# Optimization experiments

Hardware: AMD Instinct MI355X
Metric: run time of the kernel (lower is better)

## Reference

```python
import jax, jax.numpy as jnp
import numpy as np

HIDDEN = 1024
INTER = 4096
NUM_EXPERTS = 8
TOP_K = 2
LN_EPS = 1e-5


def setup_inputs() -> dict:
    key = jax.random.key(0)
    ks = jax.random.split(key, 8)
    B, S = 4, 2048
    scale = 0.02
    return {
        "hidden_states": jax.random.normal(ks[0], (B, S, HIDDEN), dtype=jnp.float32),
        "ln_scale": jnp.ones((HIDDEN,), jnp.float32),
        "ln_bias": jnp.zeros((HIDDEN,), jnp.float32),
        "router_w": jax.random.normal(ks[1], (NUM_EXPERTS, HIDDEN), jnp.float32) * scale,
        "router_b": jnp.zeros((NUM_EXPERTS,), jnp.float32),
        "up_w": jax.random.normal(ks[2], (NUM_EXPERTS, INTER, HIDDEN), jnp.float32) * scale,
        "up_b": jnp.zeros((NUM_EXPERTS, INTER), jnp.float32),
        "down_w": jax.random.normal(ks[3], (NUM_EXPERTS, HIDDEN, INTER), jnp.float32) * scale,
        "down_b": jnp.zeros((NUM_EXPERTS, HIDDEN), jnp.float32),
    }


def reference(hidden_states, ln_scale, ln_bias, router_w, router_b, up_w, up_b, down_w, down_b):
    B, S, H = hidden_states.shape
    x = hidden_states.reshape(-1, H)  # [T, H]

    # router LayerNorm (eps=1e-5, affine)
    mu = jnp.mean(x, axis=-1, keepdims=True)
    var = jnp.var(x, axis=-1, keepdims=True)
    xn = (x - mu) * jax.lax.rsqrt(var + LN_EPS) * ln_scale + ln_bias

    logits = xn @ router_w.T + router_b                # [T, E]
    top_w, top_idx = jax.lax.top_k(logits, TOP_K)      # [T, K]
    top_w = jax.nn.softmax(top_w.astype(jnp.float32), axis=-1).astype(x.dtype)

    out = jnp.zeros_like(x)
    for e in range(NUM_EXPERTS):
        # per-token combine weight for expert e (0 if not selected)
        gate = jnp.sum(jnp.where(top_idx == e, top_w, 0.0), axis=-1)  # [T]
        # expert MLP (dropout is identity in eval); GELU is exact (erf) as nn.GELU default
        h = jax.nn.gelu(x @ up_w[e].T + up_b[e], approximate=False)
        h = h @ down_w[e].T + down_b[e]
        out = out + gate[:, None] * h
    return out.reshape(B, S, H)
```

## Files before the change

kernel.cpp:

```cpp
#include <hip/hip_runtime.h>
#include <math.h>

#define HIDDEN 1024
#define INTER 4096
#define NE 8

typedef __bf16 bf16;
typedef __bf16 bf16x8 __attribute__((ext_vector_type(8)));
typedef float f32x4 __attribute__((ext_vector_type(4)));

#define WS_CTRL   ((size_t)0)
#define WS_PERM   ((size_t)256)
#define WS_GATES  ((size_t)65792)
#define WS_EIDX   ((size_t)131328)
#define WS_EGATE  ((size_t)196864)
#define WS_XB     ((size_t)262400)
#define WS_UPWB   ((size_t)17039616)
#define WS_DOWNWB ((size_t)84148480)
#define WS_H      ((size_t)151257344)
#define WS_T2S    ((size_t)285475072)
#define WS_Y      WS_UPWB

__device__ __forceinline__ void async_copy16(const void* g, void* l) {
  __builtin_amdgcn_global_load_lds((const __attribute__((address_space(1))) void*)g,
                                   (__attribute__((address_space(3))) void*)l, 16, 0, 0);
}

__device__ __forceinline__ int xcd_remap(int orig, int nwg) {
  int q = nwg >> 3, r = nwg & 7;
  int xcd = orig & 7, idx = orig >> 3;
  int base = (xcd < r) ? xcd * (q + 1) : r * (q + 1) + (xcd - r) * q;
  return base + idx;
}

__device__ __forceinline__ float gelu_erf(float v) {
  float x = v * 0.70710678118654752440f;
  float ax = fabsf(x);
  float t = __builtin_amdgcn_rcpf(fmaf(0.3275911f, ax, 1.0f));
  float p = fmaf(t, 1.061405429f, -1.453152027f);
  p = fmaf(p, t, 1.421413741f);
  p = fmaf(p, t, -0.284496736f);
  p = fmaf(p, t, 0.254829592f);
  p = p * t;
  float e = __expf(-x * x);
  float er = 1.0f - p * e;
  er = copysignf(er, x);
  return 0.5f * v * (1.0f + er);
}

__global__ void cvt_kernel(const float* __restrict__ w, bf16* __restrict__ wb, int n4) {
  int i = blockIdx.x * blockDim.x + threadIdx.x;
  int stride = gridDim.x * blockDim.x;
  for (; i < n4; i += stride) {
    float4 v = ((const float4*)w)[i];
    union { bf16 b[4]; uint2 u; } cv;
    cv.b[0] = (bf16)v.x; cv.b[1] = (bf16)v.y; cv.b[2] = (bf16)v.z; cv.b[3] = (bf16)v.w;
    ((uint2*)wb)[i] = cv.u;
  }
}

__global__ __launch_bounds__(256)
void router_kernel(const float* __restrict__ x, const float* __restrict__ lns,
                   const float* __restrict__ lnb, const float* __restrict__ rw,
                   const float* __restrict__ rb, bf16* __restrict__ xb,
                   int* __restrict__ eidx, float* __restrict__ egate) {
  const int lane = threadIdx.x & 63;
  const int wid = threadIdx.x >> 6;
  const int t = blockIdx.x * 4 + wid;
  const float4* xr = (const float4*)(x + (size_t)t * HIDDEN);
  float4 v[4];
  float s = 0.f, ss = 0.f;
#pragma unroll
  for (int q = 0; q < 4; ++q) {
    v[q] = xr[q * 64 + lane];
    s += v[q].x + v[q].y + v[q].z + v[q].w;
    ss += v[q].x * v[q].x + v[q].y * v[q].y + v[q].z * v[q].z + v[q].w * v[q].w;
  }
#pragma unroll
  for (int o = 32; o; o >>= 1) { s += __shfl_xor(s, o, 64); ss += __shfl_xor(ss, o, 64); }
  const float mu = s * (1.f / HIDDEN);
  const float rstd = rsqrtf(ss * (1.f / HIDDEN) - mu * mu + 1e-5f);
  float acc[NE] = {};
#pragma unroll
  for (int q = 0; q < 4; ++q) {
    int i4 = q * 64 + lane;
    float4 xv = v[q];
    float4 sc = ((const float4*)lns)[i4];
    float4 bi = ((const float4*)lnb)[i4];
    float4 xn;
    xn.x = (xv.x - mu) * rstd * sc.x + bi.x;
    xn.y = (xv.y - mu) * rstd * sc.y + bi.y;
    xn.z = (xv.z - mu) * rstd * sc.z + bi.z;
    xn.w = (xv.w - mu) * rstd * sc.w + bi.w;
#pragma unroll
    for (int e2 = 0; e2 < NE; ++e2) {
      float4 w = ((const float4*)(rw + e2 * HIDDEN))[i4];
      acc[e2] += xn.x * w.x + xn.y * w.y + xn.z * w.z + xn.w * w.w;
    }
    union { bf16 b[4]; uint2 u; } cv;
    cv.b[0] = (bf16)xv.x; cv.b[1] = (bf16)xv.y; cv.b[2] = (bf16)xv.z; cv.b[3] = (bf16)xv.w;
    *(uint2*)&xb[(size_t)t * HIDDEN + i4 * 4] = cv.u;
  }
#pragma unroll
  for (int e2 = 0; e2 < NE; ++e2)
#pragma unroll
    for (int o = 32; o; o >>= 1) acc[e2] += __shfl_xor(acc[e2], o, 64);
  if (lane == 0) {
    float b0 = -1e30f, b1 = -1e30f; int i0 = 0, i1 = 0;
#pragma unroll
    for (int e2 = 0; e2 < NE; ++e2) {
      float lv = acc[e2] + rb[e2];
      if (lv > b0) { b1 = b0; i1 = i0; b0 = lv; i0 = e2; }
      else if (lv > b1) { b1 = lv; i1 = e2; }
    }
    float ex = expf(b1 - b0);
    float g0 = 1.f / (1.f + ex);
    float g1 = ex * g0;
    eidx[t * 2] = i0; eidx[t * 2 + 1] = i1;
    egate[t * 2] = g0; egate[t * 2 + 1] = g1;
  }
}

__global__ __launch_bounds__(256)
void hist_kernel(const int* __restrict__ eidx, int* __restrict__ cnt) {
  __shared__ int h8[NE];
  if (threadIdx.x < NE) h8[threadIdx.x] = 0;
  __syncthreads();
  int i = (blockIdx.x * 256 + threadIdx.x) * 4;
#pragma unroll
  for (int k = 0; k < 4; ++k) atomicAdd(&h8[eidx[i + k]], 1);
  __syncthreads();
  if (threadIdx.x < NE) atomicAdd(&cnt[threadIdx.x], h8[threadIdx.x]);
}

__global__ void scan_kernel(const int* cnt, int* offs) {
  if (threadIdx.x == 0 && blockIdx.x == 0) {
    int a = 0;
    for (int e = 0; e < NE; ++e) { offs[e] = a; a += cnt[e]; }
    offs[NE] = a;
  }
}

__global__ __launch_bounds__(256)
void scatter_kernel(const int* __restrict__ eidx, const float* __restrict__ egate,
                    const int* __restrict__ offs, int* __restrict__ fill,
                    int* __restrict__ perm, float* __restrict__ gates,
                    int* __restrict__ t2s) {
  __shared__ int h8[NE], base8[NE];
  if (threadIdx.x < NE) h8[threadIdx.x] = 0;
  __syncthreads();
  int i = (blockIdx.x * 256 + threadIdx.x) * 4;
  int ee[4], rk[4];
#pragma unroll
  for (int k = 0; k < 4; ++k) { ee[k] = eidx[i + k]; rk[k] = atomicAdd(&h8[ee[k]], 1); }
  __syncthreads();
  if (threadIdx.x < NE) base8[threadIdx.x] = atomicAdd(&fill[threadIdx.x], h8[threadIdx.x]);
  __syncthreads();
#pragma unroll
  for (int k = 0; k < 4; ++k) {
    int entry = i + k;
    int slot = offs[ee[k]] + base8[ee[k]] + rk[k];
    perm[slot] = entry >> 1;
    gates[slot] = egate[entry];
    t2s[entry] = slot;
  }
}

#define READ_A(hh, cb) { \
  _Pragma("unroll") for (int ii = 0; ii < 4; ++ii) \
  _Pragma("unroll") for (int ks = 0; ks < 2; ++ks) { \
    int r_ = wr * 128 + (hh) * 64 + ii * 16 + l15; \
    af[ii][ks] = *(const bf16x8*)&sA[cb][r_ * 64 + (((ks * 4 + l16) ^ (r_ & 7)) * 8)]; \
  } }

#define READ_B(jh, cb) { \
  _Pragma("unroll") for (int jj = 0; jj < 2; ++jj) \
  _Pragma("unroll") for (int ks = 0; ks < 2; ++ks) { \
    int n_ = wc * 64 + ((jh) * 2 + jj) * 16 + l15; \
    bfr[jh][jj][ks] = *(const bf16x8*)&sB[cb][n_ * 64 + (((ks * 4 + l16) ^ (n_ & 7)) * 8)]; \
  } }

#define STAGE_A(ha, nb) { \
  async_copy16(ga[ha][0], &sA[nb][la[ha][0]]); \
  async_copy16(ga[ha][1], &sA[nb][la[ha][1]]); \
  ga[ha][0] += 64; ga[ha][1] += 64; }

#define STAGE_B(hb, nb) { \
  async_copy16(gb[hb][0], &sB[nb][lb[hb][0]]); \
  async_copy16(gb[hb][1], &sB[nb][lb[hb][1]]); \
  gb[hb][0] += 64; gb[hb][1] += 64; }

#define MFMA_CLUSTER(I0, JH) \
  __builtin_amdgcn_s_barrier(); \
  asm volatile("s_waitcnt lgkmcnt(0)" ::: "memory"); \
  __builtin_amdgcn_sched_barrier(0); \
  __builtin_amdgcn_s_setprio(1); \
  { _Pragma("unroll") for (int ii = 0; ii < 4; ++ii) \
    _Pragma("unroll") for (int jj = 0; jj < 2; ++jj) \
    _Pragma("unroll") for (int ks = 0; ks < 2; ++ks) \
      acc[(I0) + ii][(JH) * 2 + jj] = __builtin_amdgcn_mfma_f32_16x16x32_bf16( \
          af[ii][ks], bfr[JH][jj][ks], acc[(I0) + ii][(JH) * 2 + jj], 0, 0, 0); } \
  __builtin_amdgcn_s_setprio(0); \
  __builtin_amdgcn_sched_barrier(0); \
  __builtin_amdgcn_s_barrier();

#define VMW(n) asm volatile("s_waitcnt vmcnt(" #n ")" ::: "memory");

#define GEMM8_MAIN_LOOP(NT) \
  STAGE_A(0, 0); STAGE_B(0, 0); STAGE_B(1, 0); STAGE_A(1, 0); \
  VMW(4); \
  __builtin_amdgcn_s_barrier(); \
  for (int t = 0; t < (NT) - 1; ++t) { \
    const int cb = t & 1, nb = cb ^ 1; \
    READ_A(0, cb); READ_B(0, cb); \
    STAGE_A(0, nb); \
    VMW(4); \
    MFMA_CLUSTER(0, 0); \
    READ_B(1, cb); \
    STAGE_B(0, nb); \
    VMW(4); \
    MFMA_CLUSTER(0, 1); \
    READ_A(1, cb); \
    STAGE_B(1, nb); \
    MFMA_CLUSTER(4, 1); \
    STAGE_A(1, nb); \
    VMW(4); \
    MFMA_CLUSTER(4, 0); \
  } \
  { \
    const int cb = ((NT) - 1) & 1; \
    READ_A(0, cb); READ_B(0, cb); \
    VMW(0); \
    MFMA_CLUSTER(0, 0); \
    READ_B(1, cb); \
    MFMA_CLUSTER(0, 1); \
    READ_A(1, cb); \
    MFMA_CLUSTER(4, 1); \
    MFMA_CLUSTER(4, 0); \
  }

#define UP_CT (INTER / 256)
#define UP_RT 32
__global__ __launch_bounds__(512, 2)
void up_gemm8(const bf16* __restrict__ xb, const bf16* __restrict__ wb,
              const float* __restrict__ upb, const int* __restrict__ perm,
              const int* __restrict__ offs, bf16* __restrict__ h) {
  const int wgid = xcd_remap(blockIdx.x, UP_CT * UP_RT * NE);
  const int ct = wgid % UP_CT;
  const int rt = (wgid / UP_CT) % UP_RT;
  const int e  = wgid / (UP_CT * UP_RT);
  const int pbase = offs[e];
  const int ne = offs[e + 1] - pbase;
  if (rt * 256 >= ne) return;
  __shared__ __align__(16) bf16 sA[2][256 * 64];
  __shared__ __align__(16) bf16 sB[2][256 * 64];
  const int tid = threadIdx.x;
  const int lane = tid & 63;
  const int wid = tid >> 6;
  const int wr = wid >> 2;
  const int wc = wid & 3;
  const int l15 = lane & 15, l16 = lane >> 4;

  const bf16* ga[2][2]; int la[2][2];
  const bf16* gb[2][2]; int lb[2][2];
  {
    int tr = tid >> 3, tc = tid & 7;
#pragma unroll
    for (int hh = 0; hh < 2; ++hh)
#pragma unroll
      for (int l = 0; l < 2; ++l) {
        int arow = hh * 64 + tr + l * 128;
        int asch = tc ^ (arow & 7);
        int ar = rt * 256 + arow; if (ar > ne - 1) ar = ne - 1;
        int tok = perm[pbase + ar];
        ga[hh][l] = xb + (size_t)tok * HIDDEN + asch * 8;
        la[hh][l] = arow * 64 + tc * 8;
        int rl = l * 64 + tr;
        int brow = hh * 32 + (rl & 31) + (rl >> 5) * 64;
        int bsch = tc ^ (brow & 7);
        int bn = ct * 256 + brow;
        gb[hh][l] = wb + ((size_t)e * INTER + bn) * HIDDEN + bsch * 8;
        lb[hh][l] = brow * 64 + tc * 8;
      }
  }

  f32x4 acc[8][4] = {};
  bf16x8 af[4][2];
  bf16x8 bfr[2][2][2];

  GEMM8_MAIN_LOOP(HIDDEN / 64)

#pragma unroll
  for (int j4 = 0; j4 < 4; ++j4) {
    int c = ct * 256 + wc * 64 + j4 * 16 + l15;
    float bias = upb[e * INTER + c];
#pragma unroll
    for (int i8 = 0; i8 < 8; ++i8) {
#pragma unroll
      for (int tq = 0; tq < 4; ++tq) {
        int r = rt * 256 + wr * 128 + i8 * 16 + l16 * 4 + tq;
        if (r < ne) {
          float v = gelu_erf(acc[i8][j4][tq] + bias);
          h[(size_t)(pbase + r) * INTER + c] = (bf16)v;
        }
      }
    }
  }
}

#define DN_CT (HIDDEN / 256)
#define DN_RT 32
__global__ __launch_bounds__(512, 2)
void down_gemm8(const bf16* __restrict__ hh_, const bf16* __restrict__ wb,
                const float* __restrict__ dnb, const float* __restrict__ gates,
                const int* __restrict__ offs, float* __restrict__ y) {
  const int wgid = xcd_remap(blockIdx.x, DN_CT * DN_RT * NE);
  const int ct = wgid % DN_CT;
  const int rt = (wgid / DN_CT) % DN_RT;
  const int e  = wgid / (DN_CT * DN_RT);
  const int pbase = offs[e];
  const int ne = offs[e + 1] - pbase;
  if (rt * 256 >= ne) return;
  __shared__ __align__(16) bf16 sA[2][256 * 64];
  __shared__ __align__(16) bf16 sB[2][256 * 64];
  const int tid = threadIdx.x;
  const int lane = tid & 63;
  const int wid = tid >> 6;
  const int wr = wid >> 2;
  const int wc = wid & 3;
  const int l15 = lane & 15, l16 = lane >> 4;

  const bf16* ga[2][2]; int la[2][2];
  const bf16* gb[2][2]; int lb[2][2];
  {
    int tr = tid >> 3, tc = tid & 7;
#pragma unroll
    for (int hhp = 0; hhp < 2; ++hhp)
#pragma unroll
      for (int l = 0; l < 2; ++l) {
        int arow = hhp * 64 + tr + l * 128;
        int asch = tc ^ (arow & 7);
        int ar = rt * 256 + arow; if (ar > ne - 1) ar = ne - 1;
        ga[hhp][l] = hh_ + (size_t)(pbase + ar) * INTER + asch * 8;
        la[hhp][l] = arow * 64 + tc * 8;
        int rl = l * 64 + tr;
        int brow = hhp * 32 + (rl & 31) + (rl >> 5) * 64;
        int bsch = tc ^ (brow & 7);
        int bn = ct * 256 + brow;
        gb[hhp][l] = wb + ((size_t)e * HIDDEN + bn) * INTER + bsch * 8;
        lb[hhp][l] = brow * 64 + tc * 8;
      }
  }

  f32x4 acc[8][4] = {};
  bf16x8 af[4][2];
  bf16x8 bfr[2][2][2];

  GEMM8_MAIN_LOOP(INTER / 64)

  float bias[4];
#pragma unroll
  for (int j4 = 0; j4 < 4; ++j4)
    bias[j4] = dnb[e * HIDDEN + ct * 256 + wc * 64 + j4 * 16 + l15];

#pragma unroll
  for (int i8 = 0; i8 < 8; ++i8) {
#pragma unroll
    for (int tq = 0; tq < 4; ++tq) {
      int r = rt * 256 + wr * 128 + i8 * 16 + l16 * 4 + tq;
      if (r < ne) {
        int slot = pbase + r;
        float gt = gates[slot];
#pragma unroll
        for (int j4 = 0; j4 < 4; ++j4) {
          int c = ct * 256 + wc * 64 + j4 * 16 + l15;
          y[(size_t)slot * HIDDEN + c] = gt * (acc[i8][j4][tq] + bias[j4]);
        }
      }
    }
  }
}

__global__ __launch_bounds__(256)
void combine_kernel(const float* __restrict__ y, const int* __restrict__ t2s,
                    float* __restrict__ out) {
  int t = blockIdx.x;
  int s0 = t2s[2 * t], s1 = t2s[2 * t + 1];
  const float4* a = (const float4*)(y + (size_t)s0 * HIDDEN);
  const float4* b = (const float4*)(y + (size_t)s1 * HIDDEN);
  float4* o = (float4*)(out + (size_t)t * HIDDEN);
  int c = threadIdx.x;
  float4 va = a[c], vb = b[c];
  o[c] = make_float4(va.x + vb.x, va.y + vb.y, va.z + vb.z, va.w + vb.w);
}

extern "C" void kernel_launch(void* const* d_in, const int* in_sizes, int n_in,
                              void* d_out, int out_size, void* d_ws, size_t ws_size,
                              hipStream_t stream) {
  const float* x   = (const float*)d_in[0];
  const float* lns = (const float*)d_in[1];
  const float* lnb = (const float*)d_in[2];
  const float* rw  = (const float*)d_in[3];
  const float* rb  = (const float*)d_in[4];
  const float* upw = (const float*)d_in[5];
  const float* upb = (const float*)d_in[6];
  const float* dww = (const float*)d_in[7];
  const float* dwb = (const float*)d_in[8];
  float* out = (float*)d_out;

  char* ws = (char*)d_ws;
  int* ctrl   = (int*)(ws + WS_CTRL);
  int* cnt    = ctrl;
  int* fill   = ctrl + 8;
  int* offs   = ctrl + 16;
  int* perm   = (int*)(ws + WS_PERM);
  float* gates = (float*)(ws + WS_GATES);
  int* eidx   = (int*)(ws + WS_EIDX);
  float* egate = (float*)(ws + WS_EGATE);
  bf16* xb    = (bf16*)(ws + WS_XB);
  bf16* upwb  = (bf16*)(ws + WS_UPWB);
  bf16* dwwb  = (bf16*)(ws + WS_DOWNWB);
  bf16* h     = (bf16*)(ws + WS_H);
  int* t2s    = (int*)(ws + WS_T2S);
  float* y    = (float*)(ws + WS_Y);

  const int T = in_sizes[0] / HIDDEN;

  hipMemsetAsync(ctrl, 0, 256, stream);

  cvt_kernel<<<4096, 256, 0, stream>>>(upw, upwb, NE * INTER * HIDDEN / 4);
  cvt_kernel<<<4096, 256, 0, stream>>>(dww, dwwb, NE * HIDDEN * INTER / 4);
  router_kernel<<<T / 4, 256, 0, stream>>>(x, lns, lnb, rw, rb, xb, eidx, egate);
  hist_kernel<<<(2 * T) / 1024, 256, 0, stream>>>(eidx, cnt);
  scan_kernel<<<1, 64, 0, stream>>>(cnt, offs);
  scatter_kernel<<<(2 * T) / 1024, 256, 0, stream>>>(eidx, egate, offs, fill, perm, gates, t2s);

  up_gemm8<<<UP_CT * UP_RT * NE, 512, 0, stream>>>(xb, upwb, upb, perm, offs, h);
  down_gemm8<<<DN_CT * DN_RT * NE, 512, 0, stream>>>(h, dwwb, dwb, gates, offs, y);
  combine_kernel<<<T, 256, 0, stream>>>(y, t2s, out);
}
```

Measured before the change: 624.2 us.

## Double-buffer MFMA fragments and overlap LDS reads with MFMA clusters

Restructures the GEMM main loop so A/B fragments go into separate register buffers (af0/af1, b0/b1). LDS reads for the next sub-block are issued while the current MFMA block runs, and the next tile's first fragments are prefetched at the end of each iteration. Each MFMA cluster now uses one barrier instead of two and drops the explicit lgkmcnt(0) wait, and the vmcnt waits are loosened from 4 to 2. The aim is to hide LDS latency and cut barrier overhead. The cost is more VGPRs under launch_bounds(512,2), and the looser waits and barriers add a risk of races on the double-buffered shared tiles.

```diff
diff --git a/kernel.cpp b/kernel.cpp
--- a/kernel.cpp
+++ b/kernel.cpp
@@ -166,18 +166,18 @@
   }
 }
 
-#define READ_A(hh, cb) { \
+#define READ_A_TO(dst, hh, cb) { \
   _Pragma("unroll") for (int ii = 0; ii < 4; ++ii) \
   _Pragma("unroll") for (int ks = 0; ks < 2; ++ks) { \
     int r_ = wr * 128 + (hh) * 64 + ii * 16 + l15; \
-    af[ii][ks] = *(const bf16x8*)&sA[cb][r_ * 64 + (((ks * 4 + l16) ^ (r_ & 7)) * 8)]; \
+    dst[ii][ks] = *(const bf16x8*)&sA[cb][r_ * 64 + (((ks * 4 + l16) ^ (r_ & 7)) * 8)]; \
   } }
 
-#define READ_B(jh, cb) { \
+#define READ_B_TO(dst, jh, cb) { \
   _Pragma("unroll") for (int jj = 0; jj < 2; ++jj) \
   _Pragma("unroll") for (int ks = 0; ks < 2; ++ks) { \
     int n_ = wc * 64 + ((jh) * 2 + jj) * 16 + l15; \
-    bfr[jh][jj][ks] = *(const bf16x8*)&sB[cb][n_ * 64 + (((ks * 4 + l16) ^ (n_ & 7)) * 8)]; \
+    dst[jj][ks] = *(const bf16x8*)&sB[cb][n_ * 64 + (((ks * 4 + l16) ^ (n_ & 7)) * 8)]; \
   } }
 
 #define STAGE_A(ha, nb) { \
@@ -190,53 +190,58 @@
   async_copy16(gb[hb][1], &sB[nb][lb[hb][1]]); \
   gb[hb][0] += 64; gb[hb][1] += 64; }
 
-#define MFMA_CLUSTER(I0, JH) \
-  __builtin_amdgcn_s_barrier(); \
-  asm volatile("s_waitcnt lgkmcnt(0)" ::: "memory"); \
-  __builtin_amdgcn_sched_barrier(0); \
+#define MFMA_BLK(I0, JH, A, B) \
   __builtin_amdgcn_s_setprio(1); \
   { _Pragma("unroll") for (int ii = 0; ii < 4; ++ii) \
     _Pragma("unroll") for (int jj = 0; jj < 2; ++jj) \
     _Pragma("unroll") for (int ks = 0; ks < 2; ++ks) \
       acc[(I0) + ii][(JH) * 2 + jj] = __builtin_amdgcn_mfma_f32_16x16x32_bf16( \
-          af[ii][ks], bfr[JH][jj][ks], acc[(I0) + ii][(JH) * 2 + jj], 0, 0, 0); } \
-  __builtin_amdgcn_s_setprio(0); \
-  __builtin_amdgcn_sched_barrier(0); \
-  __builtin_amdgcn_s_barrier();
+          A[ii][ks], B[jj][ks], acc[(I0) + ii][(JH) * 2 + jj], 0, 0, 0); } \
+  __builtin_amdgcn_s_setprio(0);
 
 #define VMW(n) asm volatile("s_waitcnt vmcnt(" #n ")" ::: "memory");
+#define BAR() { __builtin_amdgcn_s_barrier(); __builtin_amdgcn_sched_barrier(0); }
 
 #define GEMM8_MAIN_LOOP(NT) \
   STAGE_A(0, 0); STAGE_B(0, 0); STAGE_B(1, 0); STAGE_A(1, 0); \
-  VMW(4); \
-  __builtin_amdgcn_s_barrier(); \
+  VMW(2); \
+  BAR(); \
+  READ_A_TO(af0, 0, 0); READ_B_TO(b0, 0, 0); \
   for (int t = 0; t < (NT) - 1; ++t) { \
     const int cb = t & 1, nb = cb ^ 1; \
-    READ_A(0, cb); READ_B(0, cb); \
+     \
+    READ_B_TO(b1, 1, cb); \
     STAGE_A(0, nb); \
-    VMW(4); \
-    MFMA_CLUSTER(0, 0); \
-    READ_B(1, cb); \
+    VMW(2); \
+    MFMA_BLK(0, 0, af0, b0); \
+    BAR(); \
+     \
+    READ_A_TO(af1, 1, cb); \
     STAGE_B(0, nb); \
-    VMW(4); \
-    MFMA_CLUSTER(0, 1); \
-    READ_A(1, cb); \
+    MFMA_BLK(0, 1, af0, b1); \
+    BAR(); \
+     \
     STAGE_B(1, nb); \
-    MFMA_CLUSTER(4, 1); \
+    MFMA_BLK(4, 1, af1, b1); \
+    BAR(); \
+     \
     STAGE_A(1, nb); \
-    VMW(4); \
-    MFMA_CLUSTER(4, 0); \
+    VMW(2); \
+    MFMA_BLK(4, 0, af1, b0); \
+    BAR(); \
+     \
+    READ_A_TO(af0, 0, nb); READ_B_TO(b0, 0, nb); \
   } \
-  { \
+  {  \
     const int cb = ((NT) - 1) & 1; \
-    READ_A(0, cb); READ_B(0, cb); \
+    READ_B_TO(b1, 1, cb); \
     VMW(0); \
-    MFMA_CLUSTER(0, 0); \
-    READ_B(1, cb); \
-    MFMA_CLUSTER(0, 1); \
-    READ_A(1, cb); \
-    MFMA_CLUSTER(4, 1); \
-    MFMA_CLUSTER(4, 0); \
+    BAR(); \
+    MFMA_BLK(0, 0, af0, b0); \
+    READ_A_TO(af1, 1, cb); \
+    MFMA_BLK(0, 1, af0, b1); \
+    MFMA_BLK(4, 1, af1, b1); \
+    MFMA_BLK(4, 0, af1, b0); \
   }
 
 #define UP_CT (INTER / 256)
@@ -285,8 +290,8 @@
   }
 
   f32x4 acc[8][4] = {};
-  bf16x8 af[4][2];
-  bf16x8 bfr[2][2][2];
+  bf16x8 af0[4][2], af1[4][2];
+  bf16x8 b0[2][2], b1[2][2];
 
   GEMM8_MAIN_LOOP(HIDDEN / 64)
 
@@ -353,8 +358,8 @@
   }
 
   f32x4 acc[8][4] = {};
-  bf16x8 af[4][2];
-  bf16x8 bfr[2][2][2];
+  bf16x8 af0[4][2], af1[4][2];
+  bf16x8 b0[2][2], b1[2][2];
 
   GEMM8_MAIN_LOOP(INTER / 64)
 
```

Result: slower. 904.7 us (+44.9%).
